# Optimization experiments

Measured on AMD Instinct MI355X. Metric: run time of the kernel, lower is better.

Reference implementation:

```python
import jax, jax.numpy as jnp
import numpy as np

WIN = 7
K1 = 0.01
K2 = 0.03
COV_NORM = WIN * WIN / (WIN * WIN - 1.0)  # unbiased covariance correction


def _box_filter(t):
    # t: [B, 1, H, W]; valid conv with uniform 7x7 window (mean filter)
    w = jnp.ones((1, 1, WIN, WIN), t.dtype) / (WIN * WIN)
    return jax.lax.conv_general_dilated(
        t, w, window_strides=(1, 1), padding='VALID',
        dimension_numbers=('NCHW', 'OIHW', 'NCHW'))


def setup_inputs() -> dict:
    key = jax.random.key(0)
    kx, ky = jax.random.split(key)
    B, C, H, W = 64, 1, 384, 384
    X = jax.random.normal(kx, (B, C, H, W), dtype=jnp.float32)
    Y = jax.random.normal(ky, (B, C, H, W), dtype=jnp.float32)
    data_range = jnp.ones((B,), dtype=jnp.float32)
    return {"X": X, "Y": Y, "data_range": data_range}


def reference(X, Y, data_range):
    ux = _box_filter(X)
    uy = _box_filter(Y)
    uxx = _box_filter(X * X)
    uxy = _box_filter(X * Y)
    uyy = _box_filter(Y * Y)

    vx = COV_NORM * (uxx - ux * ux)
    vy = COV_NORM * (uyy - uy * uy)
    vxy = COV_NORM * (uxy - ux * uy)

    L = data_range.reshape(-1, 1, 1, 1)  # per-sample dynamic range
    C1 = (K1 * L) ** 2
    C2 = (K2 * L) ** 2

    N1 = 2.0 * ux * uy + C1
    N2 = 2.0 * vxy + C2
    D1 = ux * ux + uy * uy + C1
    D2 = vx + vy + C2
    S = (N1 * N2) / (D1 * D2)

    # original: mean SSIM per sample, then mean over batch; equal-size maps so
    # this equals the mean over the per-sample means
    per_sample = jnp.mean(S, axis=(1, 2, 3))
    return 1.0 - jnp.mean(per_sample)
```

## Files before the change

### kernel.cpp

```cpp
#include <hip/hip_runtime.h>

#define IMH 384
#define IMW 384
#define OH 378
#define OW 378
#define NB 64
#define SROWS 21
#define INROWS 27
#define NSTRIP 18
#define BLOCK 256
#define GSTRIDE 26
#define NPAIR 14
#define SLOTF 512


template <int CTRL>
__device__ __forceinline__ float dpp_sh(float v) {
    return __int_as_float(__builtin_amdgcn_update_dpp(
        0, __float_as_int(v), CTRL, 0xf, 0xf, true));
}

__device__ __forceinline__ float2 f2add(float2 a, float2 b) { return make_float2(a.x + b.x, a.y + b.y); }
__device__ __forceinline__ float2 f2sub(float2 a, float2 b) { return make_float2(a.x - b.x, a.y - b.y); }
__device__ __forceinline__ float2 f2mul(float2 a, float2 b) { return make_float2(a.x * b.x, a.y * b.y); }
__device__ __forceinline__ float2 f2fma(float2 a, float2 b, float2 c) {
    return make_float2(fmaf(a.x, b.x, c.x), fmaf(a.y, b.y, c.y));
}
__device__ __forceinline__ float2 f2fnma(float2 a, float2 b, float2 c) {
    return make_float2(fmaf(-a.x, b.x, c.x), fmaf(-a.y, b.y, c.y));
}
__device__ __forceinline__ float2 f2fms(float2 a, float s, float2 c) {
    return make_float2(fmaf(a.x, s, -c.x), fmaf(a.y, s, -c.y));
}
__device__ __forceinline__ float2 f2s(float s) { return make_float2(s, s); }

__device__ __forceinline__ void stage16(const float* g, float* l) {
    __builtin_amdgcn_global_load_lds(
        (const __attribute__((address_space(1))) uint32_t*)(g),
        (__attribute__((address_space(3))) uint32_t*)(l),
        16, 0, 0);
}

#define WAITV(n) asm volatile("s_waitcnt vmcnt(" #n ")" ::: "memory")
#define RAWBAR() asm volatile("s_barrier" ::: "memory")

__global__ __launch_bounds__(BLOCK)
__attribute__((amdgpu_waves_per_eu(5, 8)))
void ssim_kernel(
    const float* __restrict__ X, const float* __restrict__ Y,
    const float* __restrict__ data_range, float* __restrict__ partials)
{
    const int tid   = threadIdx.x;
    const int g     = tid >> 4;
    const int j     = tid & 15;
    const int strip = blockIdx.x;
    const int b     = blockIdx.y;
    const int y0    = strip * SROWS;

    __shared__ float sX[4][2][SLOTF];
    __shared__ float sY[4][2][SLOTF];

    const int wv   = tid >> 6;
    const int ln   = tid & 63;
    const bool isX = (wv < 2);
    const int half = wv & 1;
    const int foff = half * 256 + ln * 4;
    const int fcl  = min(foff, IMW - 4);
    const float* __restrict__ gstg =
        (isX ? X : Y) + b * (IMH * IMW) + y0 * IMW + fcl;
    const float* __restrict__ gstg27 =
        (isX ? X : Y) + b * (IMH * IMW) + min(y0 + 27, IMH - 1) * IMW + fcl;
    float* const lbase = (isX ? &sX[0][0][0] : &sY[0][0][0]) + foff;

    const int ce  = g * GSTRIDE + 2 * j;
    const int cin = min(ce, IMW - 2);
    const float2 vmask = make_float2(
        ((j <= 12) && (ce     < OW)) ? 1.f : 0.f,
        ((j <= 12) && (ce + 1 < OW)) ? 1.f : 0.f);

    const float L  = data_range[b];
    const float C1 = (0.01f * L) * (0.01f * L);
    const float C2 = (0.03f * L) * (0.03f * L);
    asm volatile("" :: "v"(C1), "v"(C2));
    __builtin_amdgcn_sched_barrier(0);

    #pragma unroll
    for (int q = 0; q < 4; ++q) {
        stage16(gstg + (2 * q) * IMW,     lbase + (2 * q + 0) * SLOTF);
        stage16(gstg + (2 * q + 1) * IMW, lbase + (2 * q + 1) * SLOTF);
    }
    WAITV(6);
    RAWBAR();
    float2 cx0 = *(const float2*)&sX[0][0][cin];
    float2 cx1 = *(const float2*)&sX[0][1][cin];
    float2 cy0 = *(const float2*)&sY[0][0][cin];
    float2 cy1 = *(const float2*)&sY[0][1][cin];

    const float inv49 = 1.0f / 49.0f;
    const float covn  = 49.0f / 48.0f;

    float2 xh[7], yh[7];
    #pragma unroll
    for (int k = 0; k < 7; ++k) { xh[k] = f2s(0.f); yh[k] = f2s(0.f); }
    float2 V0 = f2s(0.f), V1 = f2s(0.f), V2 = f2s(0.f),
           V3 = f2s(0.f), V4 = f2s(0.f);
    float2 ls2 = f2s(0.f);

    auto rowcompute = [&](int r, float2 x, float2 y) {
        const int ks = r % 7;
        const float2 xo = xh[ks], yo = yh[ks];
        V0 = f2add(V0, f2sub(x, xo));
        V1 = f2add(V1, f2sub(y, yo));
        V2 = f2fma(x, x, V2);  V2 = f2fnma(xo, xo, V2);
        V3 = f2fma(x, y, V3);  V3 = f2fnma(xo, yo, V3);
        V4 = f2fma(y, y, V4);  V4 = f2fnma(yo, yo, V4);
        xh[ks] = x; yh[ks] = y;

        if (r >= 6) {
            const float2 Vv[5] = {V0, V1, V2, V3, V4};
            float Se[5], So[5];
            #pragma unroll
            for (int q = 0; q < 5; ++q) {
                const float e  = Vv[q].x;
                const float o  = Vv[q].y;
                const float pp = e + o;
                float B = pp + dpp_sh<0x101>(pp);
                float C = B + dpp_sh<0x102>(B);
                Se[q] = C - dpp_sh<0x103>(o);
                So[q] = C - e;
            }
            const float2 S0 = make_float2(Se[0], So[0]);
            const float2 S1 = make_float2(Se[1], So[1]);
            const float2 S2 = make_float2(Se[2], So[2]);
            const float2 S3 = make_float2(Se[3], So[3]);
            const float2 S4 = make_float2(Se[4], So[4]);

            float2 ux   = f2mul(S0, f2s(inv49));
            float2 uy   = f2mul(S1, f2s(inv49));
            float2 uxux = f2mul(ux, ux);
            float2 uyuy = f2mul(uy, uy);
            float2 uxuy = f2mul(ux, uy);
            float2 vx   = f2mul(f2fms(S2, inv49, uxux), f2s(covn));
            float2 vy   = f2mul(f2fms(S4, inv49, uyuy), f2s(covn));
            float2 vxy  = f2mul(f2fms(S3, inv49, uxuy), f2s(covn));
            float2 N1   = f2fma(f2s(2.f), uxuy, f2s(C1));
            float2 N2   = f2fma(f2s(2.f), vxy, f2s(C2));
            float2 D1   = f2add(f2add(uxux, uyuy), f2s(C1));
            float2 D2   = f2add(f2add(vx, vy), f2s(C2));
            float2 num  = f2mul(N1, N2);
            float2 den  = f2mul(D1, D2);
            const float rdd = __builtin_amdgcn_rcpf(den.x * den.y);
            float2 s2 = make_float2(num.x * den.y * rdd,
                                    num.y * den.x * rdd);
            ls2 = f2fma(s2, vmask, ls2);
        }
    };

    static_assert(INROWS == 27 && NPAIR == 14, "ladder");

    #pragma unroll
    for (int p = 1; p < NPAIR; ++p) {
        if      (p <= 11) WAITV(4);
        else if (p == 12) WAITV(2);
        else              WAITV(0);
        RAWBAR();

        const int sl = p & 3;
        float2 nx0 = *(const float2*)&sX[sl][0][cin];
        float2 nx1 = *(const float2*)&sX[sl][1][cin];
        float2 ny0 = *(const float2*)&sY[sl][0][cin];
        float2 ny1 = *(const float2*)&sY[sl][1][cin];

        rowcompute(2 * (p - 1),     cx0, cy0);
        rowcompute(2 * (p - 1) + 1, cx1, cy1);

        if (p + 3 < NPAIR) {
            const int q = p + 3;
            const float* s1 = (q == 13) ? gstg27 : gstg + (2 * q + 1) * IMW;
            stage16(gstg + (2 * q) * IMW, lbase + ((q & 3) * 2 + 0) * SLOTF);
            stage16(s1,                   lbase + ((q & 3) * 2 + 1) * SLOTF);
        }

        cx0 = nx0; cx1 = nx1; cy0 = ny0; cy1 = ny1;
    }

    rowcompute(26, cx0, cy0);

    float lsum = ls2.x + ls2.y;
    #pragma unroll
    for (int off = 32; off > 0; off >>= 1)
        lsum += __shfl_down(lsum, off, 64);
    __syncthreads();
    if ((tid & 63) == 0) sX[0][0][tid >> 6] = lsum;
    __syncthreads();
    if (tid == 0) {
        partials[b * NSTRIP + strip] =
            sX[0][0][0] + sX[0][0][1] + sX[0][0][2] + sX[0][0][3];
    }
}

__global__ void finalize_kernel(const float* __restrict__ partials,
                                float* __restrict__ out)
{
    float v = 0.f;
    #pragma unroll
    for (int k = 0; k < NSTRIP; ++k)
        v += partials[threadIdx.x + 64 * k];
    #pragma unroll
    for (int off = 32; off > 0; off >>= 1)
        v += __shfl_down(v, off, 64);
    if (threadIdx.x == 0)
        out[0] = 1.0f - v * (1.0f / (float)(NB * OH * OW));
}

extern "C" void kernel_launch(void* const* d_in, const int* in_sizes, int n_in,
                              void* d_out, int out_size, void* d_ws, size_t ws_size,
                              hipStream_t stream) {
    const float* X  = (const float*)d_in[0];
    const float* Y  = (const float*)d_in[1];
    const float* dr = (const float*)d_in[2];
    float* out = (float*)d_out;
    float* partials = (float*)d_ws;

    dim3 grid(NSTRIP, NB);
    dim3 block(BLOCK);
    ssim_kernel<<<grid, block, 0, stream>>>(X, Y, dr, partials);
    finalize_kernel<<<1, 64, 0, stream>>>(partials, out);
}
```

Before: 27.93 us.

## Fuse final reduction via last-block atomic, shrink strips, simplify SSIM algebra

Replaces the separate finalize kernel with a last-block-done atomic counter that reduces partials inside the main kernel, resetting the counter with a memset. Strips shrink from 21 to 18 output rows (more blocks, smaller LDS slots with overlapping half-row staging), and the per-pixel SSIM formula is rewritten on unscaled sums with folded constants to cut multiplies. Trades extra halo-row reloads and an atomic/fence tail for fewer launches and less ALU work.

```diff
diff --git a/kernel.cpp b/kernel.cpp
--- a/kernel.cpp
+++ b/kernel.cpp
@@ -5,13 +5,14 @@
 #define OH 378
 #define OW 378
 #define NB 64
-#define SROWS 21
-#define INROWS 27
-#define NSTRIP 18
+#define SROWS 18
+#define INROWS 24
+#define NSTRIP 21
 #define BLOCK 256
 #define GSTRIDE 26
-#define NPAIR 14
-#define SLOTF 512
+#define NPAIR 12
+#define SLOTF 384
+#define NBLK (NSTRIP * NB)
 
 
 template <int CTRL>
@@ -48,7 +49,8 @@
 __attribute__((amdgpu_waves_per_eu(5, 8)))
 void ssim_kernel(
     const float* __restrict__ X, const float* __restrict__ Y,
-    const float* __restrict__ data_range, float* __restrict__ partials)
+    const float* __restrict__ data_range, float* __restrict__ partials,
+    float* __restrict__ out)
 {
     const int tid   = threadIdx.x;
     const int g     = tid >> 4;
@@ -59,18 +61,16 @@
 
     __shared__ float sX[4][2][SLOTF];
     __shared__ float sY[4][2][SLOTF];
+    __shared__ int lastflag;
 
     const int wv   = tid >> 6;
     const int ln   = tid & 63;
     const bool isX = (wv < 2);
     const int half = wv & 1;
-    const int foff = half * 256 + ln * 4;
-    const int fcl  = min(foff, IMW - 4);
+    const int foff = half * 128 + ln * 4;
     const float* __restrict__ gstg =
-        (isX ? X : Y) + b * (IMH * IMW) + y0 * IMW + fcl;
-    const float* __restrict__ gstg27 =
-        (isX ? X : Y) + b * (IMH * IMW) + min(y0 + 27, IMH - 1) * IMW + fcl;
-    float* const lbase = (isX ? &sX[0][0][0] : &sY[0][0][0]) + foff;
+        (isX ? X : Y) + b * (IMH * IMW) + y0 * IMW + foff;
+    float* const lbase = (isX ? &sX[0][0][0] : &sY[0][0][0]) + half * 128;
 
     const int ce  = g * GSTRIDE + 2 * j;
     const int cin = min(ce, IMW - 2);
@@ -78,10 +78,12 @@
         ((j <= 12) && (ce     < OW)) ? 1.f : 0.f,
         ((j <= 12) && (ce + 1 < OW)) ? 1.f : 0.f);
 
-    const float L  = data_range[b];
-    const float C1 = (0.01f * L) * (0.01f * L);
-    const float C2 = (0.03f * L) * (0.03f * L);
-    asm volatile("" :: "v"(C1), "v"(C2));
+    const float L   = data_range[b];
+    const float c1s = (0.49f * L) * (0.49f * L);
+    const float c2s = (1.47f * L) * (1.47f * L);
+    const float k1  = 49.0f / 48.0f;
+    const float k2  = 49.0f / 24.0f;
+    asm volatile("" :: "v"(c1s), "v"(c2s));
     __builtin_amdgcn_sched_barrier(0);
 
     #pragma unroll
@@ -95,9 +97,6 @@
     float2 cx1 = *(const float2*)&sX[0][1][cin];
     float2 cy0 = *(const float2*)&sY[0][0][cin];
     float2 cy1 = *(const float2*)&sY[0][1][cin];
-
-    const float inv49 = 1.0f / 49.0f;
-    const float covn  = 49.0f / 48.0f;
 
     float2 xh[7], yh[7];
     #pragma unroll
@@ -135,20 +134,18 @@
             const float2 S3 = make_float2(Se[3], So[3]);
             const float2 S4 = make_float2(Se[4], So[4]);
 
-            float2 ux   = f2mul(S0, f2s(inv49));
-            float2 uy   = f2mul(S1, f2s(inv49));
-            float2 uxux = f2mul(ux, ux);
-            float2 uyuy = f2mul(uy, uy);
-            float2 uxuy = f2mul(ux, uy);
-            float2 vx   = f2mul(f2fms(S2, inv49, uxux), f2s(covn));
-            float2 vy   = f2mul(f2fms(S4, inv49, uyuy), f2s(covn));
-            float2 vxy  = f2mul(f2fms(S3, inv49, uxuy), f2s(covn));
-            float2 N1   = f2fma(f2s(2.f), uxuy, f2s(C1));
-            float2 N2   = f2fma(f2s(2.f), vxy, f2s(C2));
-            float2 D1   = f2add(f2add(uxux, uyuy), f2s(C1));
-            float2 D2   = f2add(f2add(vx, vy), f2s(C2));
-            float2 num  = f2mul(N1, N2);
-            float2 den  = f2mul(D1, D2);
+            float2 P  = f2mul(S0, S1);
+            float2 q1 = f2mul(S1, S1);
+            float2 QQ = f2fma(S0, S0, q1);
+            float2 N1 = f2fma(f2s(2.f), P, f2s(c1s));
+            float2 D1 = f2add(QQ, f2s(c1s));
+            float2 w  = f2fms(S3, 49.0f, P);
+            float2 N2 = f2fma(f2s(k2), w, f2s(c2s));
+            float2 t  = f2add(S2, S4);
+            float2 u  = f2fms(t, 49.0f, QQ);
+            float2 D2 = f2fma(f2s(k1), u, f2s(c2s));
+            float2 num = f2mul(N1, N2);
+            float2 den = f2mul(D1, D2);
             const float rdd = __builtin_amdgcn_rcpf(den.x * den.y);
             float2 s2 = make_float2(num.x * den.y * rdd,
                                     num.y * den.x * rdd);
@@ -156,12 +153,12 @@
         }
     };
 
-    static_assert(INROWS == 27 && NPAIR == 14, "ladder");
+    static_assert(INROWS == 24 && NPAIR == 12, "ladder");
 
     #pragma unroll
     for (int p = 1; p < NPAIR; ++p) {
-        if      (p <= 11) WAITV(4);
-        else if (p == 12) WAITV(2);
+        if      (p <= 9)  WAITV(4);
+        else if (p == 10) WAITV(2);
         else              WAITV(0);
         RAWBAR();
 
@@ -176,15 +173,15 @@
 
         if (p + 3 < NPAIR) {
             const int q = p + 3;
-            const float* s1 = (q == 13) ? gstg27 : gstg + (2 * q + 1) * IMW;
-            stage16(gstg + (2 * q) * IMW, lbase + ((q & 3) * 2 + 0) * SLOTF);
-            stage16(s1,                   lbase + ((q & 3) * 2 + 1) * SLOTF);
+            stage16(gstg + (2 * q) * IMW,     lbase + ((q & 3) * 2 + 0) * SLOTF);
+            stage16(gstg + (2 * q + 1) * IMW, lbase + ((q & 3) * 2 + 1) * SLOTF);
         }
 
         cx0 = nx0; cx1 = nx1; cy0 = ny0; cy1 = ny1;
     }
 
-    rowcompute(26, cx0, cy0);
+    rowcompute(22, cx0, cy0);
+    rowcompute(23, cx1, cy1);
 
     float lsum = ls2.x + ls2.y;
     #pragma unroll
@@ -194,23 +191,27 @@
     if ((tid & 63) == 0) sX[0][0][tid >> 6] = lsum;
     __syncthreads();
     if (tid == 0) {
-        partials[b * NSTRIP + strip] =
-            sX[0][0][0] + sX[0][0][1] + sX[0][0][2] + sX[0][0][3];
-    }
-}
-
-__global__ void finalize_kernel(const float* __restrict__ partials,
-                                float* __restrict__ out)
-{
-    float v = 0.f;
-    #pragma unroll
-    for (int k = 0; k < NSTRIP; ++k)
-        v += partials[threadIdx.x + 64 * k];
-    #pragma unroll
-    for (int off = 32; off > 0; off >>= 1)
-        v += __shfl_down(v, off, 64);
-    if (threadIdx.x == 0)
-        out[0] = 1.0f - v * (1.0f / (float)(NB * OH * OW));
+        const float bs = sX[0][0][0] + sX[0][0][1]
+                       + sX[0][0][2] + sX[0][0][3];
+        partials[b * NSTRIP + strip] = bs;
+        __threadfence();
+        const unsigned old =
+            atomicAdd((unsigned*)(partials + NBLK), 1u);
+        lastflag = (old == NBLK - 1) ? 1 : 0;
+    }
+    __syncthreads();
+    if (lastflag && tid < 64) {
+        __threadfence();
+        float v = 0.f;
+        #pragma unroll
+        for (int k = 0; k < NBLK / 64; ++k)
+            v += atomicAdd(partials + tid + 64 * k, 0.0f);
+        #pragma unroll
+        for (int off = 32; off > 0; off >>= 1)
+            v += __shfl_down(v, off, 64);
+        if (tid == 0)
+            out[0] = 1.0f - v * (1.0f / (float)(NB * OH * OW));
+    }
 }
 
 extern "C" void kernel_launch(void* const* d_in, const int* in_sizes, int n_in,
@@ -222,8 +223,10 @@
     float* out = (float*)d_out;
     float* partials = (float*)d_ws;
 
+    hipMemsetAsync((char*)d_ws + NBLK * sizeof(float), 0, sizeof(unsigned),
+                   stream);
+
     dim3 grid(NSTRIP, NB);
     dim3 block(BLOCK);
-    ssim_kernel<<<grid, block, 0, stream>>>(X, Y, dr, partials);
-    finalize_kernel<<<1, 64, 0, stream>>>(partials, out);
-}
+    ssim_kernel<<<grid, block, 0, stream>>>(X, Y, dr, partials, out);
+}
```

Result: slower. 68.10 us (+143.8%).
